# Kernel optimization log

Hardware: AMD Instinct MI355X
Metric: run time of the kernel (lower is better)

Reference implementation:

```python
import jax, jax.numpy as jnp
import numpy as np

B, S, D, H, DK, F, L, V = 4, 128, 512, 8, 64, 2048, 2, 32000
N = B * S  # nodes per side (enc and dec each)


def _pe():
    pos = np.arange(S, dtype=np.float32)[:, None]
    div = np.exp(-np.log(10000.0) * np.arange(0, D, 2, dtype=np.float32) / D)
    pe = np.zeros((S, D), dtype=np.float32)
    pe[:, 0::2] = np.sin(pos * div)
    pe[:, 1::2] = np.cos(pos * div)
    return jnp.asarray(np.tile(pe, (B, 1)))  # [N, D]


def _ln(x, g, b, eps=1e-5):
    mu = jnp.mean(x, -1, keepdims=True)
    var = jnp.mean(jnp.square(x - mu), -1, keepdims=True)
    return g * (x - mu) * jax.lax.rsqrt(var + eps) + b


def _edge_attn(q, k, v, src, dst, n_dst):
    # src_dot_dst('k','q','score') then scaled_exp, then src_mul_edge + sum scatter
    s = jnp.sum(k[src] * q[dst], -1, keepdims=True) / np.float32(np.sqrt(DK))  # [E,H,1]
    s = jnp.exp(jnp.clip(s, -10.0, 10.0))
    wv = jax.ops.segment_sum(v[src] * s, dst, num_segments=n_dst)  # [n_dst,H,DK]
    z = jax.ops.segment_sum(s, dst, num_segments=n_dst)            # [n_dst,H,1]
    return wv / z


def _attn_block(x_q, x_kv, Wq, Wk, Wv, Wo, src, dst):
    q = (x_q @ Wq).reshape(-1, H, DK)
    k = (x_kv @ Wk).reshape(-1, H, DK)
    v = (x_kv @ Wv).reshape(-1, H, DK)
    o = _edge_attn(q, k, v, src, dst, x_q.shape[0]).reshape(-1, D)
    return o @ Wo


def _forward(p, src_tok, tgt_tok, ee_src, ee_dst, dd_src, dd_dst, ed_src, ed_dst):
    (src_emb, tgt_emb, enc_Wqkv, enc_Wo, enc_ln1, enc_W1, enc_b1, enc_W2, enc_b2,
     enc_ln2, enc_lnf, dec_Wqkv, dec_Wo, dec_ln1, dec_cWq, dec_cWkv, dec_cWo,
     dec_ln2, dec_W1, dec_b1, dec_W2, dec_b2, dec_ln3, dec_lnf, gen_W, gen_b) = p
    pe = _pe()
    scale = np.float32(np.sqrt(D))
    x_e = src_emb[src_tok].reshape(N, D) * scale + pe  # token + positional embed
    x_d = tgt_emb[tgt_tok].reshape(N, D) * scale + pe
    for l in range(L):  # encoder layers (ee edges)
        xn = _ln(x_e, enc_ln1[l, 0], enc_ln1[l, 1])
        x_e = x_e + _attn_block(xn, xn, enc_Wqkv[l, 0], enc_Wqkv[l, 1], enc_Wqkv[l, 2], enc_Wo[l], ee_src, ee_dst)
        xn = _ln(x_e, enc_ln2[l, 0], enc_ln2[l, 1])
        x_e = x_e + jax.nn.relu(xn @ enc_W1[l] + enc_b1[l]) @ enc_W2[l] + enc_b2[l]
    x_e = _ln(x_e, enc_lnf[0], enc_lnf[1])
    for l in range(L):  # decoder layers: self (dd) then cross (ed)
        xn = _ln(x_d, dec_ln1[l, 0], dec_ln1[l, 1])
        x_d = x_d + _attn_block(xn, xn, dec_Wqkv[l, 0], dec_Wqkv[l, 1], dec_Wqkv[l, 2], dec_Wo[l], dd_src, dd_dst)
        xn = _ln(x_d, dec_ln2[l, 0], dec_ln2[l, 1])
        x_d = x_d + _attn_block(xn, x_e, dec_cWq[l], dec_cWkv[l, 0], dec_cWkv[l, 1], dec_cWo[l], ed_src, ed_dst)
        xn = _ln(x_d, dec_ln3[l, 0], dec_ln3[l, 1])
        x_d = x_d + jax.nn.relu(xn @ dec_W1[l] + dec_b1[l]) @ dec_W2[l] + dec_b2[l]
    x_d = _ln(x_d, dec_lnf[0], dec_lnf[1])
    return jax.nn.log_softmax(x_d @ gen_W + gen_b, axis=-1)  # generator


def setup_inputs():
    key = jax.random.key(0)
    ks = iter(jax.random.split(key, 32))
    w = lambda *shape: jax.random.normal(next(ks), shape, jnp.float32) * 0.02
    lnp = lambda n: jnp.tile(jnp.stack([jnp.ones(D), jnp.zeros(D)])[None], (n, 1, 1))
    # structured edge lists: per-sentence blocks
    i, j = np.meshgrid(np.arange(S), np.arange(S), indexing='ij')  # src pos, dst pos
    base = (np.arange(B)[:, None] * S).astype(np.int32)
    full_s = (base + i.ravel()[None, :]).ravel().astype(np.int32)
    full_d = (base + j.ravel()[None, :]).ravel().astype(np.int32)
    m = i.ravel() <= j.ravel()  # causal mask for dec self-attention
    dd_s = (base + i.ravel()[m][None, :]).ravel().astype(np.int32)
    dd_d = (base + j.ravel()[m][None, :]).ravel().astype(np.int32)
    k1, k2 = jax.random.split(next(ks))
    return dict(
        src_emb=w(V, D), tgt_emb=w(V, D),
        enc_Wqkv=w(L, 3, D, D), enc_Wo=w(L, D, D), enc_ln1=lnp(L),
        enc_W1=w(L, D, F), enc_b1=jnp.zeros((L, F)), enc_W2=w(L, F, D),
        enc_b2=jnp.zeros((L, D)), enc_ln2=lnp(L), enc_lnf=lnp(1)[0],
        dec_Wqkv=w(L, 3, D, D), dec_Wo=w(L, D, D), dec_ln1=lnp(L),
        dec_cWq=w(L, D, D), dec_cWkv=w(L, 2, D, D), dec_cWo=w(L, D, D), dec_ln2=lnp(L),
        dec_W1=w(L, D, F), dec_b1=jnp.zeros((L, F)), dec_W2=w(L, F, D),
        dec_b2=jnp.zeros((L, D)), dec_ln3=lnp(L), dec_lnf=lnp(1)[0],
        gen_W=w(D, V), gen_b=jnp.zeros((V,)),
        src_tok=jax.random.randint(k1, (B, S), 0, V, jnp.int32),
        tgt_tok=jax.random.randint(k2, (B, S), 0, V, jnp.int32),
        ee_src=jnp.asarray(full_s), ee_dst=jnp.asarray(full_d),
        dd_src=jnp.asarray(dd_s), dd_dst=jnp.asarray(dd_d),
        ed_src=jnp.asarray(full_s), ed_dst=jnp.asarray(full_d),
    )


def reference(src_emb, tgt_emb, enc_Wqkv, enc_Wo, enc_ln1, enc_W1, enc_b1, enc_W2,
              enc_b2, enc_ln2, enc_lnf, dec_Wqkv, dec_Wo, dec_ln1, dec_cWq,
              dec_cWkv, dec_cWo, dec_ln2, dec_W1, dec_b1, dec_W2, dec_b2,
              dec_ln3, dec_lnf, gen_W, gen_b, src_tok, tgt_tok, ee_src, ee_dst,
              dd_src, dd_dst, ed_src, ed_dst):
    p = (src_emb, tgt_emb, enc_Wqkv, enc_Wo, enc_ln1, enc_W1, enc_b1, enc_W2,
         enc_b2, enc_ln2, enc_lnf, dec_Wqkv, dec_Wo, dec_ln1, dec_cWq, dec_cWkv,
         dec_cWo, dec_ln2, dec_W1, dec_b1, dec_W2, dec_b2, dec_ln3, dec_lnf,
         gen_W, gen_b)
    return _forward(p, src_tok, tgt_tok, ee_src, ee_dst, dd_src, dd_dst, ed_src, ed_dst)
```

## Files before the change

kernel.cpp:

```cpp
#include <hip/hip_runtime.h>
#include <cstddef>

constexpr int cB = 4, cS = 128, cD = 512, cH = 8, cDK = 64, cF = 2048, cL = 2, cV = 32000;
constexpr int cN = cB * cS;

typedef __attribute__((ext_vector_type(8))) short short8;
typedef __attribute__((ext_vector_type(4))) float f32x4;

__device__ __forceinline__ short f2bf(float x) {
    unsigned u = __builtin_bit_cast(unsigned, x);
    unsigned r = (u + 0x7fffu + ((u >> 16) & 1u)) >> 16;
    return (short)r;
}

__global__ __launch_bounds__(256) void embed_k(const float* __restrict__ emb,
                                               const int* __restrict__ tok,
                                               float* __restrict__ X)
{
    int n = blockIdx.x;
    int tid = threadIdx.x;
    int t = tok[n];
    int pos = n & (cS - 1);
    const float scale = 22.62741699796952f;
    for (int d = tid; d < cD; d += 256) {
        int i2 = d & ~1;
        float div = expf(-9.210340371976184f * (float)i2 / (float)cD);
        float arg = (float)pos * div;
        float p = (d & 1) ? cosf(arg) : sinf(arg);
        X[(long)n * cD + d] = emb[(long)t * cD + d] * scale + p;
    }
}

__global__ __launch_bounds__(256) void ln_k(const float* __restrict__ X,
                                            const float* __restrict__ g,
                                            const float* __restrict__ bta,
                                            short* __restrict__ Yb)
{
    __shared__ float red[256];
    int row = blockIdx.x, tid = threadIdx.x;
    const float* x = X + (long)row * cD;
    float v0 = x[tid], v1 = x[tid + 256];

    red[tid] = v0 + v1;
    __syncthreads();
    for (int st = 128; st > 0; st >>= 1) { if (tid < st) red[tid] += red[tid + st]; __syncthreads(); }
    float mu = red[0] * (1.0f / (float)cD);
    __syncthreads();

    float d0 = v0 - mu, d1 = v1 - mu;
    red[tid] = d0 * d0 + d1 * d1;
    __syncthreads();
    for (int st = 128; st > 0; st >>= 1) { if (tid < st) red[tid] += red[tid + st]; __syncthreads(); }
    float var = red[0] * (1.0f / (float)cD);
    float rs = rsqrtf(var + 1e-5f);

    Yb[(long)row * cD + tid]       = f2bf(g[tid]       * d0 * rs + bta[tid]);
    Yb[(long)row * cD + tid + 256] = f2bf(g[tid + 256] * d1 * rs + bta[tid + 256]);
}

struct TCP { const float* s[24]; };

__global__ __launch_bounds__(256) void tconv_k(TCP ptrs, short* __restrict__ dst,
                                               int K, int N)
{
    __shared__ float t[64][65];
    const float* s = ptrs.s[blockIdx.z];
    short* d = dst + (long)blockIdx.z * K * N;
    int k0 = blockIdx.y * 64, n0 = blockIdx.x * 64;
    int tid = threadIdx.x;
    const f32x4* s4 = (const f32x4*)s;
#pragma unroll
    for (int i = 0; i < 4; i++) {
        int lin = tid + i * 256;
        int r = lin >> 4, c4 = lin & 15;
        f32x4 v = s4[(long)(k0 + r) * (N >> 2) + (n0 >> 2) + c4];
        t[r][c4 * 4 + 0] = v[0]; t[r][c4 * 4 + 1] = v[1];
        t[r][c4 * 4 + 2] = v[2]; t[r][c4 * 4 + 3] = v[3];
    }
    __syncthreads();
#pragma unroll
    for (int i = 0; i < 2; i++) {
        int lin = tid + i * 256;
        int r = lin >> 3, c8 = lin & 7;
        short8 o;
#pragma unroll
        for (int j = 0; j < 8; j++) o[j] = f2bf(t[c8 * 8 + j][r]);
        *(short8*)&d[(long)(n0 + r) * K + k0 + c8 * 8] = o;
    }
}

template <int MR, int NR, bool LNF>
__global__ __launch_bounds__(256) void gemm_k(
    const short* __restrict__ Abf, const float* __restrict__ Af,
    const float* __restrict__ lng, const float* __restrict__ lnb,
    const short* __restrict__ Bt,
    const float* __restrict__ bias, const float* __restrict__ res,
    float* __restrict__ C, short* __restrict__ Cb,
    int N, int K, int relu, long btStride, long cStride, int swz)
{
    constexpr int BM = MR * 32, BN = NR * 32, BK = 64, PITCH = BK + 8;
    constexpr int ACH = (BM * BK) / (8 * 256);
    constexpr int BCH = (BN * BK) / (8 * 256);
    static_assert(ACH >= 1 && BCH >= 1, "tile too small");
    __shared__ short As[2][BM * PITCH];
    __shared__ short Bs[2][BN * PITCH];
    __shared__ float mu_s[BM], rs_s[BM];
    __shared__ float gb_s[2][512];

    int bx = blockIdx.x, by = blockIdx.y;
    if (swz) {
        int nb = gridDim.x * gridDim.y;
        int bid = by * gridDim.x + bx;
        int w = (bid & 7) * (nb >> 3) + (bid >> 3);
        by = w % gridDim.y; bx = w / gridDim.y;
    }

    const short* Bm = Bt + (long)blockIdx.z * btStride;
    int tid = threadIdx.x;
    int lane = tid & 63, wid = tid >> 6;
    int wr = wid >> 1, wc = wid & 1;
    int m0 = by * BM, n0 = bx * BN;
    int lrow = lane & 15, koff = (lane >> 4) * 8;

    f32x4 acc[MR][NR];
#pragma unroll
    for (int m = 0; m < MR; m++)
#pragma unroll
        for (int n = 0; n < NR; n++) acc[m][n] = f32x4{0.f, 0.f, 0.f, 0.f};

    short8 qa0[ACH], qa1[ACH], qb0[BCH], qb1[BCH];
    f32x4 fa0[LNF ? ACH * 2 : 1], fa1[LNF ? ACH * 2 : 1];

    auto stageA = [&](int k0, short8 (&qa)[ACH], f32x4 (&fa)[LNF ? ACH * 2 : 1]) {
#pragma unroll
        for (int i = 0; i < ACH; i++) {
            int lin = tid + i * 256, r = lin >> 3, c8 = lin & 7;
            if constexpr (LNF) {
                const f32x4* p = (const f32x4*)(Af + (long)(m0 + r) * K + k0 + c8 * 8);
                fa[2 * i] = p[0]; fa[2 * i + 1] = p[1];
            } else {
                qa[i] = *(const short8*)&Abf[(long)(m0 + r) * K + k0 + c8 * 8];
            }
        }
    };
    auto stageB = [&](int k0, short8 (&qb)[BCH]) {
#pragma unroll
        for (int i = 0; i < BCH; i++) {
            int lin = tid + i * 256, r = lin >> 3, c8 = lin & 7;
            qb[i] = *(const short8*)&Bm[(long)(n0 + r) * K + k0 + c8 * 8];
        }
    };
    auto writeT = [&](int buf, int k0, short8 (&qa)[ACH],
                      f32x4 (&fa)[LNF ? ACH * 2 : 1], short8 (&qb)[BCH]) {
#pragma unroll
        for (int i = 0; i < ACH; i++) {
            int lin = tid + i * 256, r = lin >> 3, c8 = lin & 7;
            if constexpr (LNF) {
                float mu = mu_s[r], rs = rs_s[r];
                short8 o;
#pragma unroll
                for (int j = 0; j < 4; j++)
                    o[j] = f2bf((fa[2 * i][j] - mu) * rs * gb_s[0][k0 + c8 * 8 + j] + gb_s[1][k0 + c8 * 8 + j]);
#pragma unroll
                for (int j = 0; j < 4; j++)
                    o[4 + j] = f2bf((fa[2 * i + 1][j] - mu) * rs * gb_s[0][k0 + c8 * 8 + 4 + j] + gb_s[1][k0 + c8 * 8 + 4 + j]);
                *(short8*)&As[buf][r * PITCH + c8 * 8] = o;
            } else {
                *(short8*)&As[buf][r * PITCH + c8 * 8] = qa[i];
            }
        }
#pragma unroll
        for (int i = 0; i < BCH; i++) {
            int lin = tid + i * 256, r = lin >> 3, c8 = lin & 7;
            *(short8*)&Bs[buf][r * PITCH + c8 * 8] = qb[i];
        }
    };
    auto mfmaStep = [&](int buf) {
#pragma unroll
        for (int kk = 0; kk < BK; kk += 32) {
            short8 a[MR], b[NR];
#pragma unroll
            for (int m = 0; m < MR; m++)
                a[m] = *(const short8*)&As[buf][(wr * MR * 16 + m * 16 + lrow) * PITCH + kk + koff];
#pragma unroll
            for (int n = 0; n < NR; n++)
                b[n] = *(const short8*)&Bs[buf][(wc * NR * 16 + n * 16 + lrow) * PITCH + kk + koff];
#pragma unroll
            for (int m = 0; m < MR; m++)
#pragma unroll
                for (int n = 0; n < NR; n++)
                    acc[m][n] = __builtin_amdgcn_mfma_f32_16x16x32_bf16(a[m], b[n], acc[m][n], 0, 0, 0);
        }
    };

    stageA(0, qa0, fa0); stageB(0, qb0);
    if (BK < K) { stageA(BK, qa1, fa1); stageB(BK, qb1); }

    if constexpr (LNF) {
        constexpr int TPR = 256 / BM;
        int r = tid / TPR, sub = tid % TPR;
        const f32x4* row4 = (const f32x4*)(Af + (long)(m0 + r) * K);
        float s = 0.f, s2 = 0.f;
        for (int i = sub; i < (K >> 2); i += TPR) {
            f32x4 v = row4[i];
            s  += v[0] + v[1] + v[2] + v[3];
            s2 += v[0] * v[0] + v[1] * v[1] + v[2] * v[2] + v[3] * v[3];
        }
#pragma unroll
        for (int o = TPR >> 1; o > 0; o >>= 1) {
            s += __shfl_xor(s, o); s2 += __shfl_xor(s2, o);
        }
        if (sub == 0) {
            float mu = s / (float)K;
            float var = s2 / (float)K - mu * mu;
            mu_s[r] = mu; rs_s[r] = rsqrtf(var + 1e-5f);
        }
        for (int i = tid; i < 512; i += 256) {
            gb_s[0][i] = lng[i]; gb_s[1][i] = lnb[i];
        }
        __syncthreads();
    }

    int k0 = 0;
    for (;;) {
        writeT(0, k0, qa0, fa0, qb0);
        __syncthreads();
        if (k0 + 2 * BK < K) { stageA(k0 + 2 * BK, qa0, fa0); stageB(k0 + 2 * BK, qb0); }
        mfmaStep(0);
        k0 += BK; if (k0 >= K) break;

        writeT(1, k0, qa1, fa1, qb1);
        __syncthreads();
        if (k0 + 2 * BK < K) { stageA(k0 + 2 * BK, qa1, fa1); stageB(k0 + 2 * BK, qb1); }
        mfmaStep(1);
        k0 += BK; if (k0 >= K) break;
    }

#pragma unroll
    for (int m = 0; m < MR; m++) {
        int rbase = m0 + wr * MR * 16 + m * 16 + (lane >> 4) * 4;
#pragma unroll
        for (int n = 0; n < NR; n++) {
            int col = n0 + wc * NR * 16 + n * 16 + (lane & 15);
            float bv = bias ? bias[col] : 0.f;
#pragma unroll
            for (int j = 0; j < 4; j++) {
                long row = rbase + j;
                float v = acc[m][n][j] + bv;
                if (res)  v += res[row * N + col];
                if (relu) v = fmaxf(v, 0.f);
                long off = row * N + col + (long)blockIdx.z * cStride;
                if (C)  C[off] = v;
                if (Cb) Cb[off] = f2bf(v);
            }
        }
    }
}

__global__ __launch_bounds__(256) void attn_k(const short* __restrict__ Q,
                                              const short* __restrict__ Km,
                                              const short* __restrict__ Vm,
                                              short* __restrict__ O, int causal)
{
    __shared__ short q_s[64 * 72];
    __shared__ short k_s[128 * 72];
    __shared__ short vt_s[64 * 128];
    __shared__ short p_s[64 * 136];
    __shared__ float z_s[64];

    int tid = threadIdx.x, lane = tid & 63, wid = tid >> 6;
    int lr = lane & 15, lg = lane >> 4;
    int h = blockIdx.x, b = blockIdx.y, dstBase = blockIdx.z * 64;
    const int RS = cH * cDK;
    long qbase = ((long)b * cS + dstBase) * RS + h * cDK;
    long kbase = ((long)b * cS) * RS + h * cDK;

#pragma unroll
    for (int i = 0; i < 2; i++) {
        int lin = tid + i * 256, t = lin >> 3, c8 = lin & 7;
        *(short8*)&q_s[t * 72 + c8 * 8] = *(const short8*)&Q[qbase + (long)t * RS + c8 * 8];
    }
#pragma unroll
    for (int i = 0; i < 4; i++) {
        int lin = tid + i * 256, t = lin >> 3, c8 = lin & 7;
        *(short8*)&k_s[t * 72 + c8 * 8] = *(const short8*)&Km[kbase + (long)t * RS + c8 * 8];
    }
#pragma unroll
    for (int i = 0; i < 4; i++) {
        int lin = tid + i * 256, src = lin >> 3, c8 = lin & 7;
        short8 v = *(const short8*)&Vm[kbase + (long)src * RS + c8 * 8];
#pragma unroll
        for (int j = 0; j < 8; j++) {
            int dk = c8 * 8 + j;
            int g = (src >> 3) ^ (dk >> 3);
            vt_s[dk * 128 + g * 8 + (src & 7)] = v[j];
        }
    }
    __syncthreads();

    f32x4 sacc[8];
#pragma unroll
    for (int n = 0; n < 8; n++) sacc[n] = f32x4{0.f, 0.f, 0.f, 0.f};
#pragma unroll
    for (int kk = 0; kk < 64; kk += 32) {
        short8 a = *(const short8*)&q_s[(wid * 16 + lr) * 72 + kk + lg * 8];
#pragma unroll
        for (int n = 0; n < 8; n++) {
            short8 bf = *(const short8*)&k_s[(n * 16 + lr) * 72 + kk + lg * 8];
            sacc[n] = __builtin_amdgcn_mfma_f32_16x16x32_bf16(a, bf, sacc[n], 0, 0, 0);
        }
    }
    float z[4] = {0.f, 0.f, 0.f, 0.f};
#pragma unroll
    for (int n = 0; n < 8; n++) {
        int src = n * 16 + lr;
#pragma unroll
        for (int j = 0; j < 4; j++) {
            int dst = dstBase + wid * 16 + lg * 4 + j;
            float s = sacc[n][j] * 0.125f;
            s = __expf(fminf(fmaxf(s, -10.f), 10.f));
            if (causal && src > dst) s = 0.f;
            sacc[n][j] = s;
            z[j] += s;
        }
    }
#pragma unroll
    for (int j = 0; j < 4; j++) {
        z[j] += __shfl_xor(z[j], 1); z[j] += __shfl_xor(z[j], 2);
        z[j] += __shfl_xor(z[j], 4); z[j] += __shfl_xor(z[j], 8);
    }
#pragma unroll
    for (int n = 0; n < 8; n++) {
        int src = n * 16 + lr;
#pragma unroll
        for (int j = 0; j < 4; j++)
            p_s[(wid * 16 + lg * 4 + j) * 136 + src] = f2bf(sacc[n][j]);
    }
    if (lr == 0) {
#pragma unroll
        for (int j = 0; j < 4; j++) z_s[wid * 16 + lg * 4 + j] = z[j];
    }
    __syncthreads();

    f32x4 oacc[4];
#pragma unroll
    for (int n = 0; n < 4; n++) oacc[n] = f32x4{0.f, 0.f, 0.f, 0.f};
#pragma unroll
    for (int kk = 0; kk < 128; kk += 32) {
        int dkr = wid * 16 + lr;
        int g = ((kk >> 3) + lg) ^ (dkr >> 3);
        short8 a = *(const short8*)&vt_s[dkr * 128 + g * 8];
#pragma unroll
        for (int n = 0; n < 4; n++) {
            short8 bf = *(const short8*)&p_s[(n * 16 + lr) * 136 + kk + lg * 8];
            oacc[n] = __builtin_amdgcn_mfma_f32_16x16x32_bf16(a, bf, oacc[n], 0, 0, 0);
        }
    }
#pragma unroll
    for (int n = 0; n < 4; n++) {
        int dl = n * 16 + lr;
        float zz = z_s[dl];
#pragma unroll
        for (int j = 0; j < 4; j++) {
            int dk = wid * 16 + lg * 4 + j;
            O[qbase + (long)dl * RS + dk] = f2bf(oacc[n][j] / zz);
        }
    }
}

__global__ __launch_bounds__(256) void lsm_k(float* __restrict__ X)
{
    __shared__ float rm[256], rs[256];
    int row = blockIdx.x, tid = threadIdx.x;
    f32x4* x4 = (f32x4*)(X + (long)row * cV);
    constexpr int NV = cV / 4;

    float m = -1e30f, s = 0.f;
    for (int i = tid; i < NV; i += 256) {
        f32x4 v = x4[i];
        float cm = fmaxf(fmaxf(v[0], v[1]), fmaxf(v[2], v[3]));
        float nm = fmaxf(m, cm);
        s = s * __expf(m - nm)
          + __expf(v[0] - nm) + __expf(v[1] - nm)
          + __expf(v[2] - nm) + __expf(v[3] - nm);
        m = nm;
    }
    rm[tid] = m; rs[tid] = s;
    __syncthreads();
    for (int st = 128; st > 0; st >>= 1) {
        if (tid < st) {
            float m2 = rm[tid + st], s2 = rs[tid + st];
            float nm = fmaxf(rm[tid], m2);
            rs[tid] = rs[tid] * __expf(rm[tid] - nm) + s2 * __expf(m2 - nm);
            rm[tid] = nm;
        }
        __syncthreads();
    }
    float lse = rm[0] + __logf(rs[0]);

    for (int i = tid; i < NV; i += 256) {
        f32x4 v = x4[i];
        v[0] -= lse; v[1] -= lse; v[2] -= lse; v[3] -= lse;
        x4[i] = v;
    }
}

extern "C" void kernel_launch(void* const* d_in, const int* in_sizes, int n_in,
                              void* d_out, int out_size, void* d_ws, size_t ws_size,
                              hipStream_t stream)
{
    const float* src_emb  = (const float*)d_in[0];
    const float* tgt_emb  = (const float*)d_in[1];
    const float* enc_Wqkv = (const float*)d_in[2];
    const float* enc_Wo   = (const float*)d_in[3];
    const float* enc_ln1  = (const float*)d_in[4];
    const float* enc_W1   = (const float*)d_in[5];
    const float* enc_b1   = (const float*)d_in[6];
    const float* enc_W2   = (const float*)d_in[7];
    const float* enc_b2   = (const float*)d_in[8];
    const float* enc_ln2  = (const float*)d_in[9];
    const float* enc_lnf  = (const float*)d_in[10];
    const float* dec_Wqkv = (const float*)d_in[11];
    const float* dec_Wo   = (const float*)d_in[12];
    const float* dec_ln1  = (const float*)d_in[13];
    const float* dec_cWq  = (const float*)d_in[14];
    const float* dec_cWkv = (const float*)d_in[15];
    const float* dec_cWo  = (const float*)d_in[16];
    const float* dec_ln2  = (const float*)d_in[17];
    const float* dec_W1   = (const float*)d_in[18];
    const float* dec_b1   = (const float*)d_in[19];
    const float* dec_W2   = (const float*)d_in[20];
    const float* dec_b2   = (const float*)d_in[21];
    const float* dec_ln3  = (const float*)d_in[22];
    const float* dec_lnf  = (const float*)d_in[23];
    const float* gen_W    = (const float*)d_in[24];
    const float* gen_b    = (const float*)d_in[25];
    const int* src_tok    = (const int*)d_in[26];
    const int* tgt_tok    = (const int*)d_in[27];

    const long ND = (long)cN * cD;
    const long DD = (long)cD * cD;
    const long DF = (long)cD * cF;

    float* x_e = (float*)d_ws;
    float* x_d = x_e + ND;

    short* qkvb  = (short*)(x_d + ND);
    short* ob_bf = qkvb + 3 * ND;
    short* hb_bf = ob_bf + ND;
    short* kvc   = hb_bf + (long)cN * cF;
    short* xn_bf = kvc + 4 * ND;
    short* wDD  = xn_bf + ND;
    short* wDF  = wDD + 24 * DD;
    short* wFD  = wDF + 4 * DF;
    short* genT = wFD + 4 * DF;

    {
        TCP p{};
        int i = 0;
        for (int j = 0; j < 6; j++) p.s[i++] = enc_Wqkv + (long)j * DD;
        for (int j = 0; j < 2; j++) p.s[i++] = enc_Wo   + (long)j * DD;
        for (int j = 0; j < 6; j++) p.s[i++] = dec_Wqkv + (long)j * DD;
        for (int j = 0; j < 2; j++) p.s[i++] = dec_Wo   + (long)j * DD;
        for (int j = 0; j < 2; j++) p.s[i++] = dec_cWq  + (long)j * DD;
        for (int j = 0; j < 4; j++) p.s[i++] = dec_cWkv + (long)j * DD;
        for (int j = 0; j < 2; j++) p.s[i++] = dec_cWo  + (long)j * DD;
        tconv_k<<<dim3(cD / 64, cD / 64, 24), 256, 0, stream>>>(p, wDD, cD, cD);
    }
    {
        TCP p{};
        p.s[0] = enc_W1; p.s[1] = enc_W1 + DF; p.s[2] = dec_W1; p.s[3] = dec_W1 + DF;
        tconv_k<<<dim3(cF / 64, cD / 64, 4), 256, 0, stream>>>(p, wDF, cD, cF);
    }
    {
        TCP p{};
        p.s[0] = enc_W2; p.s[1] = enc_W2 + DF; p.s[2] = dec_W2; p.s[3] = dec_W2 + DF;
        tconv_k<<<dim3(cD / 64, cF / 64, 4), 256, 0, stream>>>(p, wFD, cF, cD);
    }
    {
        TCP p{};
        p.s[0] = gen_W;
        tconv_k<<<dim3(cV / 64, cD / 64, 1), 256, 0, stream>>>(p, genT, cD, cV);
    }

    embed_k<<<cN, 256, 0, stream>>>(src_emb, src_tok, x_e);
    embed_k<<<cN, 256, 0, stream>>>(tgt_emb, tgt_tok, x_d);

    dim3 gDD11(cD / 32, cN / 32);
    dim3 gFFN1(cF / 64, cN / 64);
    dim3 gAttn(cH, cB, 2);

    for (int l = 0; l < cL; l++) {
        gemm_k<1, 1, true><<<dim3(cD / 32, cN / 32, 3), 256, 0, stream>>>(
            nullptr, x_e, enc_ln1 + (long)(2 * l) * cD, enc_ln1 + (long)(2 * l + 1) * cD,
            wDD + (long)(3 * l) * DD, nullptr, nullptr, nullptr, qkvb,
            cD, cD, 0, DD, ND, 0);
        attn_k<<<gAttn, 256, 0, stream>>>(qkvb, qkvb + ND, qkvb + 2 * ND, ob_bf, 0);
        gemm_k<1, 1, false><<<gDD11, 256, 0, stream>>>(
            ob_bf, nullptr, nullptr, nullptr, wDD + (long)(6 + l) * DD,
            nullptr, x_e, x_e, nullptr, cD, cD, 0, 0, 0, 0);
        gemm_k<2, 2, true><<<gFFN1, 256, 0, stream>>>(
            nullptr, x_e, enc_ln2 + (long)(2 * l) * cD, enc_ln2 + (long)(2 * l + 1) * cD,
            wDF + (long)l * DF, enc_b1 + (long)l * cF, nullptr, nullptr, hb_bf,
            cF, cD, 1, 0, 0, 0);
        gemm_k<1, 1, false><<<gDD11, 256, 0, stream>>>(
            hb_bf, nullptr, nullptr, nullptr, wFD + (long)l * DF,
            enc_b2 + (long)l * cD, x_e, x_e, nullptr, cD, cF, 0, 0, 0, 0);
    }

    gemm_k<1, 1, true><<<dim3(cD / 32, cN / 32, 4), 256, 0, stream>>>(
        nullptr, x_e, enc_lnf, enc_lnf + cD,
        wDD + 18 * DD, nullptr, nullptr, nullptr, kvc,
        cD, cD, 0, DD, ND, 0);

    for (int l = 0; l < cL; l++) {
        gemm_k<1, 1, true><<<dim3(cD / 32, cN / 32, 3), 256, 0, stream>>>(
            nullptr, x_d, dec_ln1 + (long)(2 * l) * cD, dec_ln1 + (long)(2 * l + 1) * cD,
            wDD + (long)(8 + 3 * l) * DD, nullptr, nullptr, nullptr, qkvb,
            cD, cD, 0, DD, ND, 0);
        attn_k<<<gAttn, 256, 0, stream>>>(qkvb, qkvb + ND, qkvb + 2 * ND, ob_bf, 1);
        gemm_k<1, 1, false><<<gDD11, 256, 0, stream>>>(
            ob_bf, nullptr, nullptr, nullptr, wDD + (long)(14 + l) * DD,
            nullptr, x_d, x_d, nullptr, cD, cD, 0, 0, 0, 0);

        gemm_k<1, 1, true><<<gDD11, 256, 0, stream>>>(
            nullptr, x_d, dec_ln2 + (long)(2 * l) * cD, dec_ln2 + (long)(2 * l + 1) * cD,
            wDD + (long)(16 + l) * DD, nullptr, nullptr, nullptr, qkvb,
            cD, cD, 0, 0, 0, 0);
        attn_k<<<gAttn, 256, 0, stream>>>(qkvb, kvc + (long)(2 * l) * ND,
                                          kvc + (long)(2 * l + 1) * ND, ob_bf, 0);
        gemm_k<1, 1, false><<<gDD11, 256, 0, stream>>>(
            ob_bf, nullptr, nullptr, nullptr, wDD + (long)(22 + l) * DD,
            nullptr, x_d, x_d, nullptr, cD, cD, 0, 0, 0, 0);

        gemm_k<2, 2, true><<<gFFN1, 256, 0, stream>>>(
            nullptr, x_d, dec_ln3 + (long)(2 * l) * cD, dec_ln3 + (long)(2 * l + 1) * cD,
            wDF + (long)(2 + l) * DF, dec_b1 + (long)l * cF, nullptr, nullptr, hb_bf,
            cF, cD, 1, 0, 0, 0);
        gemm_k<1, 1, false><<<gDD11, 256, 0, stream>>>(
            hb_bf, nullptr, nullptr, nullptr, wFD + (long)(2 + l) * DF,
            dec_b2 + (long)l * cD, x_d, x_d, nullptr, cD, cF, 0, 0, 0, 0);
    }

    ln_k<<<cN, 256, 0, stream>>>(x_d, dec_lnf, dec_lnf + cD, xn_bf);
    gemm_k<4, 2, false><<<dim3(cV / 64, cN / 128), 256, 0, stream>>>(
        xn_bf, nullptr, nullptr, nullptr, genT, gen_b, nullptr,
        (float*)d_out, nullptr, cV, cD, 0, 0, 0, 1);
    lsm_k<<<cN, 256, 0, stream>>>((float*)d_out);
}
```

Measured before the change: 377.8 us.

## Add 32x32 MFMA generator GEMM with fp16 logits, relaxed barriers, fused embed

Adds a dedicated 128x128-tile generator GEMM built on 32x32x16 bf16 MFMA that writes fp16 logits to a workspace buffer. Log-softmax now reads those half-precision logits and writes the fp32 output, so the vocab-sized intermediate traffic is roughly halved. GEMM and attention barriers are replaced by an lgkmcnt wait plus s_barrier, and the barrier is moved after the next global prefetch is issued. The two embedding launches are merged into one grid. Rounding logits to fp16 before log-softmax loses precision, and the workspace must be large enough to hold the extra logits buffer.

```diff
diff --git a/kernel.cpp b/kernel.cpp
--- a/kernel.cpp
+++ b/kernel.cpp
@@ -4,19 +4,38 @@
 constexpr int cB = 4, cS = 128, cD = 512, cH = 8, cDK = 64, cF = 2048, cL = 2, cV = 32000;
 constexpr int cN = cB * cS;
 
-typedef __attribute__((ext_vector_type(8))) short short8;
-typedef __attribute__((ext_vector_type(4))) float f32x4;
+typedef __attribute__((ext_vector_type(8)))  short short8;
+typedef __attribute__((ext_vector_type(4)))  float f32x4;
+typedef __attribute__((ext_vector_type(16))) float f32x16;
 
 __device__ __forceinline__ short f2bf(float x) {
     unsigned u = __builtin_bit_cast(unsigned, x);
     unsigned r = (u + 0x7fffu + ((u >> 16) & 1u)) >> 16;
     return (short)r;
 }
-
-__global__ __launch_bounds__(256) void embed_k(const float* __restrict__ emb,
-                                               const int* __restrict__ tok,
-                                               float* __restrict__ X)
-{
+__device__ __forceinline__ short f2h(float x) {
+    return __builtin_bit_cast(short, (_Float16)x);
+}
+__device__ __forceinline__ float h2f(short s) {
+    return (float)__builtin_bit_cast(_Float16, s);
+}
+
+__device__ __forceinline__ void bar_lgkm() {
+    asm volatile("s_waitcnt lgkmcnt(0)" ::: "memory");
+    __builtin_amdgcn_s_barrier();
+    asm volatile("" ::: "memory");
+}
+
+__global__ __launch_bounds__(256) void embed_k(const float* __restrict__ e0,
+                                               const int* __restrict__ t0,
+                                               float* __restrict__ X0,
+                                               const float* __restrict__ e1,
+                                               const int* __restrict__ t1,
+                                               float* __restrict__ X1)
+{
+    const float* emb = blockIdx.z ? e1 : e0;
+    const int* tok   = blockIdx.z ? t1 : t0;
+    float* X         = blockIdx.z ? X1 : X0;
     int n = blockIdx.x;
     int tid = threadIdx.x;
     int t = tok[n];
@@ -218,20 +237,20 @@
         for (int i = tid; i < 512; i += 256) {
             gb_s[0][i] = lng[i]; gb_s[1][i] = lnb[i];
         }
-        __syncthreads();
+        bar_lgkm();
     }
 
     int k0 = 0;
     for (;;) {
         writeT(0, k0, qa0, fa0, qb0);
-        __syncthreads();
         if (k0 + 2 * BK < K) { stageA(k0 + 2 * BK, qa0, fa0); stageB(k0 + 2 * BK, qb0); }
+        bar_lgkm();
         mfmaStep(0);
         k0 += BK; if (k0 >= K) break;
 
         writeT(1, k0, qa1, fa1, qb1);
-        __syncthreads();
         if (k0 + 2 * BK < K) { stageA(k0 + 2 * BK, qa1, fa1); stageB(k0 + 2 * BK, qb1); }
+        bar_lgkm();
         mfmaStep(1);
         k0 += BK; if (k0 >= K) break;
     }
@@ -296,7 +315,7 @@
             vt_s[dk * 128 + g * 8 + (src & 7)] = v[j];
         }
     }
-    __syncthreads();
+    bar_lgkm();
 
     f32x4 sacc[8];
 #pragma unroll
@@ -340,7 +359,7 @@
 #pragma unroll
         for (int j = 0; j < 4; j++) z_s[wid * 16 + lg * 4 + j] = z[j];
     }
-    __syncthreads();
+    bar_lgkm();
 
     f32x4 oacc[4];
 #pragma unroll
@@ -368,21 +387,135 @@
     }
 }
 
-__global__ __launch_bounds__(256) void lsm_k(float* __restrict__ X)
+__global__ __launch_bounds__(256) void gen32_k(
+    const short* __restrict__ A, const short* __restrict__ Bt,
+    const float* __restrict__ bias, short* __restrict__ Ch, int N, int K)
+{
+    constexpr int PITCH = 72;
+    constexpr int ACH = 4, BCH = 4;
+    __shared__ short As[2][128 * PITCH];
+    __shared__ short Bs[2][128 * PITCH];
+
+    int bx = blockIdx.x, by = blockIdx.y;
+    {
+        int nb = gridDim.x * gridDim.y;
+        int bid = by * gridDim.x + bx;
+        int w = (bid & 7) * (nb >> 3) + (bid >> 3);
+        by = w % gridDim.y; bx = w / gridDim.y;
+    }
+    int tid = threadIdx.x;
+    int lane = tid & 63, wid = tid >> 6;
+    int wr = wid >> 1, wc = wid & 1;
+    int m0 = by * 128, n0 = bx * 128;
+    int l31 = lane & 31, l5 = lane >> 5;
+
+    f32x16 acc[2][2];
+#pragma unroll
+    for (int m = 0; m < 2; m++)
+#pragma unroll
+        for (int n = 0; n < 2; n++)
+#pragma unroll
+            for (int r = 0; r < 16; r++) acc[m][n][r] = 0.f;
+
+    short8 qa0[ACH], qa1[ACH], qb0[BCH], qb1[BCH];
+    auto stage = [&](int k0, short8 (&qa)[ACH], short8 (&qb)[BCH]) {
+#pragma unroll
+        for (int i = 0; i < ACH; i++) {
+            int lin = tid + i * 256, r = lin >> 3, c8 = lin & 7;
+            qa[i] = *(const short8*)&A[(long)(m0 + r) * K + k0 + c8 * 8];
+        }
+#pragma unroll
+        for (int i = 0; i < BCH; i++) {
+            int lin = tid + i * 256, r = lin >> 3, c8 = lin & 7;
+            qb[i] = *(const short8*)&Bt[(long)(n0 + r) * K + k0 + c8 * 8];
+        }
+    };
+    auto writeT = [&](int buf, short8 (&qa)[ACH], short8 (&qb)[BCH]) {
+#pragma unroll
+        for (int i = 0; i < ACH; i++) {
+            int lin = tid + i * 256, r = lin >> 3, c8 = lin & 7;
+            *(short8*)&As[buf][r * PITCH + c8 * 8] = qa[i];
+        }
+#pragma unroll
+        for (int i = 0; i < BCH; i++) {
+            int lin = tid + i * 256, r = lin >> 3, c8 = lin & 7;
+            *(short8*)&Bs[buf][r * PITCH + c8 * 8] = qb[i];
+        }
+    };
+    auto mfmaStep = [&](int buf) {
+#pragma unroll
+        for (int kk = 0; kk < 64; kk += 16) {
+            short8 a[2], b[2];
+#pragma unroll
+            for (int m = 0; m < 2; m++)
+                a[m] = *(const short8*)&As[buf][(wr * 64 + m * 32 + l31) * PITCH + kk + l5 * 8];
+#pragma unroll
+            for (int n = 0; n < 2; n++)
+                b[n] = *(const short8*)&Bs[buf][(wc * 64 + n * 32 + l31) * PITCH + kk + l5 * 8];
+#pragma unroll
+            for (int m = 0; m < 2; m++)
+#pragma unroll
+                for (int n = 0; n < 2; n++)
+                    acc[m][n] = __builtin_amdgcn_mfma_f32_32x32x16_bf16(a[m], b[n], acc[m][n], 0, 0, 0);
+        }
+    };
+
+    const int steps = K >> 6;
+    stage(0, qa0, qb0);
+    stage(64, qa1, qb1);
+    int st = 0;
+    for (;;) {
+        writeT(0, qa0, qb0);
+        if (st + 2 < steps) stage((st + 2) * 64, qa0, qb0);
+        bar_lgkm();
+        mfmaStep(0);
+        st++; if (st >= steps) break;
+
+        writeT(1, qa1, qb1);
+        if (st + 2 < steps) stage((st + 2) * 64, qa1, qb1);
+        bar_lgkm();
+        mfmaStep(1);
+        st++; if (st >= steps) break;
+    }
+
+#pragma unroll
+    for (int m = 0; m < 2; m++) {
+#pragma unroll
+        for (int n = 0; n < 2; n++) {
+            int col = n0 + wc * 64 + n * 32 + l31;
+            float bv = bias[col];
+#pragma unroll
+            for (int r = 0; r < 16; r++) {
+                int row = m0 + wr * 64 + m * 32 + (r & 3) + 8 * (r >> 2) + 4 * l5;
+                Ch[(long)row * N + col] = f2h(acc[m][n][r] + bv);
+            }
+        }
+    }
+}
+
+__global__ __launch_bounds__(256) void lsm_k(const short* __restrict__ L16,
+                                             float* __restrict__ Out)
 {
     __shared__ float rm[256], rs[256];
     int row = blockIdx.x, tid = threadIdx.x;
-    f32x4* x4 = (f32x4*)(X + (long)row * cV);
-    constexpr int NV = cV / 4;
+    const short8* x8 = (const short8*)(L16 + (long)row * cV);
+    float* o = Out + (long)row * cV;
+    constexpr int NV = cV / 8;
 
     float m = -1e30f, s = 0.f;
     for (int i = tid; i < NV; i += 256) {
-        f32x4 v = x4[i];
-        float cm = fmaxf(fmaxf(v[0], v[1]), fmaxf(v[2], v[3]));
+        short8 v = x8[i];
+        float f[8];
+#pragma unroll
+        for (int j = 0; j < 8; j++) f[j] = h2f(v[j]);
+        float cm = f[0];
+#pragma unroll
+        for (int j = 1; j < 8; j++) cm = fmaxf(cm, f[j]);
         float nm = fmaxf(m, cm);
-        s = s * __expf(m - nm)
-          + __expf(v[0] - nm) + __expf(v[1] - nm)
-          + __expf(v[2] - nm) + __expf(v[3] - nm);
+        float a = 0.f;
+#pragma unroll
+        for (int j = 0; j < 8; j++) a += __expf(f[j] - nm);
+        s = s * __expf(m - nm) + a;
         m = nm;
     }
     rm[tid] = m; rs[tid] = s;
@@ -399,9 +532,14 @@
     float lse = rm[0] + __logf(rs[0]);
 
     for (int i = tid; i < NV; i += 256) {
-        f32x4 v = x4[i];
-        v[0] -= lse; v[1] -= lse; v[2] -= lse; v[3] -= lse;
-        x4[i] = v;
+        short8 v = x8[i];
+        f32x4 o0, o1;
+#pragma unroll
+        for (int j = 0; j < 4; j++) o0[j] = h2f(v[j]) - lse;
+#pragma unroll
+        for (int j = 0; j < 4; j++) o1[j] = h2f(v[4 + j]) - lse;
+        *(f32x4*)&o[i * 8]     = o0;
+        *(f32x4*)&o[i * 8 + 4] = o1;
     }
 }
 
@@ -454,6 +592,7 @@
     short* wDF  = wDD + 24 * DD;
     short* wFD  = wDF + 4 * DF;
     short* genT = wFD + 4 * DF;
+    short* lg16 = genT + (long)cD * cV;
 
     {
         TCP p{};
@@ -483,10 +622,10 @@
         tconv_k<<<dim3(cV / 64, cD / 64, 1), 256, 0, stream>>>(p, genT, cD, cV);
     }
 
-    embed_k<<<cN, 256, 0, stream>>>(src_emb, src_tok, x_e);
-    embed_k<<<cN, 256, 0, stream>>>(tgt_emb, tgt_tok, x_d);
-
-    dim3 gDD11(cD / 32, cN / 32);
+    embed_k<<<dim3(cN, 1, 2), 256, 0, stream>>>(src_emb, src_tok, x_e,
+                                                tgt_emb, tgt_tok, x_d);
+
+    dim3 gDD(cD / 32, cN / 32);
     dim3 gFFN1(cF / 64, cN / 64);
     dim3 gAttn(cH, cB, 2);
 
@@ -496,22 +635,21 @@
             wDD + (long)(3 * l) * DD, nullptr, nullptr, nullptr, qkvb,
             cD, cD, 0, DD, ND, 0);
         attn_k<<<gAttn, 256, 0, stream>>>(qkvb, qkvb + ND, qkvb + 2 * ND, ob_bf, 0);
-        gemm_k<1, 1, false><<<gDD11, 256, 0, stream>>>(
+        gemm_k<1, 1, false><<<gDD, 256, 0, stream>>>(
             ob_bf, nullptr, nullptr, nullptr, wDD + (long)(6 + l) * DD,
             nullptr, x_e, x_e, nullptr, cD, cD, 0, 0, 0, 0);
         gemm_k<2, 2, true><<<gFFN1, 256, 0, stream>>>(
             nullptr, x_e, enc_ln2 + (long)(2 * l) * cD, enc_ln2 + (long)(2 * l + 1) * cD,
             wDF + (long)l * DF, enc_b1 + (long)l * cF, nullptr, nullptr, hb_bf,
             cF, cD, 1, 0, 0, 0);
-        gemm_k<1, 1, false><<<gDD11, 256, 0, stream>>>(
+        gemm_k<1, 1, false><<<gDD, 256, 0, stream>>>(
             hb_bf, nullptr, nullptr, nullptr, wFD + (long)l * DF,
             enc_b2 + (long)l * cD, x_e, x_e, nullptr, cD, cF, 0, 0, 0, 0);
     }
 
     gemm_k<1, 1, true><<<dim3(cD / 32, cN / 32, 4), 256, 0, stream>>>(
         nullptr, x_e, enc_lnf, enc_lnf + cD,
-        wDD + 18 * DD, nullptr, nullptr, nullptr, kvc,
-        cD, cD, 0, DD, ND, 0);
+        wDD + 18 * DD, nullptr, nullptr, nullptr, kvc, cD, cD, 0, DD, ND, 0);
 
     for (int l = 0; l < cL; l++) {
         gemm_k<1, 1, true><<<dim3(cD / 32, cN / 32, 3), 256, 0, stream>>>(
@@ -519,17 +657,17 @@
             wDD + (long)(8 + 3 * l) * DD, nullptr, nullptr, nullptr, qkvb,
             cD, cD, 0, DD, ND, 0);
         attn_k<<<gAttn, 256, 0, stream>>>(qkvb, qkvb + ND, qkvb + 2 * ND, ob_bf, 1);
-        gemm_k<1, 1, false><<<gDD11, 256, 0, stream>>>(
+        gemm_k<1, 1, false><<<gDD, 256, 0, stream>>>(
             ob_bf, nullptr, nullptr, nullptr, wDD + (long)(14 + l) * DD,
             nullptr, x_d, x_d, nullptr, cD, cD, 0, 0, 0, 0);
 
-        gemm_k<1, 1, true><<<gDD11, 256, 0, stream>>>(
+        gemm_k<1, 1, true><<<gDD, 256, 0, stream>>>(
             nullptr, x_d, dec_ln2 + (long)(2 * l) * cD, dec_ln2 + (long)(2 * l + 1) * cD,
             wDD + (long)(16 + l) * DD, nullptr, nullptr, nullptr, qkvb,
             cD, cD, 0, 0, 0, 0);
         attn_k<<<gAttn, 256, 0, stream>>>(qkvb, kvc + (long)(2 * l) * ND,
                                           kvc + (long)(2 * l + 1) * ND, ob_bf, 0);
-        gemm_k<1, 1, false><<<gDD11, 256, 0, stream>>>(
+        gemm_k<1, 1, false><<<gDD, 256, 0, stream>>>(
             ob_bf, nullptr, nullptr, nullptr, wDD + (long)(22 + l) * DD,
             nullptr, x_d, x_d, nullptr, cD, cD, 0, 0, 0, 0);
 
@@ -537,14 +675,13 @@
             nullptr, x_d, dec_ln3 + (long)(2 * l) * cD, dec_ln3 + (long)(2 * l + 1) * cD,
             wDF + (long)(2 + l) * DF, dec_b1 + (long)l * cF, nullptr, nullptr, hb_bf,
             cF, cD, 1, 0, 0, 0);
-        gemm_k<1, 1, false><<<gDD11, 256, 0, stream>>>(
+        gemm_k<1, 1, false><<<gDD, 256, 0, stream>>>(
             hb_bf, nullptr, nullptr, nullptr, wFD + (long)(2 + l) * DF,
             dec_b2 + (long)l * cD, x_d, x_d, nullptr, cD, cF, 0, 0, 0, 0);
     }
 
     ln_k<<<cN, 256, 0, stream>>>(x_d, dec_lnf, dec_lnf + cD, xn_bf);
-    gemm_k<4, 2, false><<<dim3(cV / 64, cN / 128), 256, 0, stream>>>(
-        xn_bf, nullptr, nullptr, nullptr, genT, gen_b, nullptr,
-        (float*)d_out, nullptr, cV, cD, 0, 0, 0, 1);
-    lsm_k<<<cN, 256, 0, stream>>>((float*)d_out);
-}
+    gen32_k<<<dim3(cV / 128, cN / 128), 256, 0, stream>>>(
+        xn_bf, genT, gen_b, lg16, cV, cD);
+    lsm_k<<<cN, 256, 0, stream>>>(lg16, (float*)d_out);
+}
```

Measured after the change: 357.0 us. 5.5% less time.
